# Optimization experiments

Hardware: AMD Instinct MI355X
Metric: run time of the kernel (lower is better)

Reference implementation:

```python
import jax, jax.numpy as jnp
import numpy as np

B, N, D = 4, 2048, 1024
H, HD = 16, 64
S = 11  # n_scales
D4 = jnp.array([0.4829629131445341, 0.8365163037378079,
                0.2241438680420134, -0.1294095225512604], dtype=jnp.float32)


def _causal_dilated_d4(f, d):
    """Causal depthwise D4 conv with dilation d along axis 2. f: [B,H,N,HD].
    Matches torch F.pad(x,(3d,0)) + F.conv1d(dilation=d, groups=C):
    y[n] = sum_t D4[t] * f[n - (3-t)*d]."""
    n = f.shape[2]
    fp = jnp.pad(f, ((0, 0), (0, 0), (3 * d, 0), (0, 0)))
    return (D4[0] * fp[:, :, 0:n, :]
            + D4[1] * fp[:, :, d:d + n, :]
            + D4[2] * fp[:, :, 2 * d:2 * d + n, :]
            + D4[3] * fp[:, :, 3 * d:3 * d + n, :])


def setup_inputs() -> dict:
    key = jax.random.key(0)
    ks = jax.random.split(key, 10)
    s = 0.02
    return {
        "x": jax.random.normal(ks[0], (B, N, D), dtype=jnp.float32),
        "Wqkv": jax.random.normal(ks[1], (3 * D, D), dtype=jnp.float32) * s,
        "bqkv": jnp.zeros((3 * D,), dtype=jnp.float32),
        "Wo": jax.random.normal(ks[2], (D, D), dtype=jnp.float32) * s,
        "bo": jnp.zeros((D,), dtype=jnp.float32),
        "Wg": jax.random.normal(ks[3], (D, D), dtype=jnp.float32) * s,
        "bg": jnp.full((D,), 2.0, dtype=jnp.float32),
        "scale_gain": jnp.zeros((S, H), dtype=jnp.float32),
        "Wqs": jax.random.normal(ks[4], (S, HD), dtype=jnp.float32) * 0.01,
        "field_coupling": jnp.eye(H, dtype=jnp.float32)
        + 0.01 * jax.random.normal(ks[5], (H, H), dtype=jnp.float32),
    }


def reference(x, Wqkv, bqkv, Wo, bo, Wg, bg, scale_gain, Wqs, field_coupling):
    b, n, d = x.shape
    qkv = x @ Wqkv.T + bqkv                          # [B,N,3D]
    q, k, v = jnp.split(qkv, 3, axis=-1)
    q = q.reshape(b, n, H, HD).transpose(0, 2, 1, 3)  # [B,H,N,HD]
    k = k.reshape(b, n, H, HD).transpose(0, 2, 1, 3)
    v = v.reshape(b, n, H, HD).transpose(0, 2, 1, 3)

    # per-position scale gains: learned prior + query-conditioned offset
    q_offset = jnp.einsum('bhnd,sd->bhns', q, Wqs)    # [B,H,N,S]
    prior = scale_gain.T[None, :, None, :]            # [1,H,1,S]
    gains = jax.nn.softmax(q_offset + prior, axis=-1)

    # deposit: field[i] = V[i] * ||K[i]||
    k_mag = jnp.linalg.norm(k, axis=-1, keepdims=True)
    field = v * k_mag                                 # [B,H,N,HD]

    # propagate: causal multiscale dilated D4 conv, gain-weighted accumulate
    out_field = jnp.zeros_like(field)
    for j in range(S):
        y = _causal_dilated_d4(field, 1 << j)
        out_field = out_field + gains[:, :, :, j:j + 1] * y

    coupling = jax.nn.softmax(field_coupling, axis=-1)
    out_field = jnp.einsum('ij,bjnd->bind', coupling, out_field)

    gate = jax.nn.sigmoid(x @ Wg.T + bg)              # [B,N,D]
    gathered = out_field.transpose(0, 2, 1, 3).reshape(b, n, d)
    return (gathered * gate) @ Wo.T + bo
```

## Files before the change

kernel.cpp:

```cpp
#include <hip/hip_runtime.h>
#include <hip/hip_bf16.h>
#include <stdint.h>
#include <math.h>

#define BB 4
#define NN 2048
#define DD 1024
#define HH 16
#define HDD 64
#define SS 11

#define D4_0 0.4829629131445341f
#define D4_1 0.8365163037378079f
#define D4_2 0.2241438680420134f
#define D4_3 (-0.1294095225512604f)

typedef __bf16 bf16_t;
typedef __bf16 bf16x4_t __attribute__((ext_vector_type(4)));
typedef __bf16 bf16x8_t __attribute__((ext_vector_type(8)));
typedef float f32x4_t __attribute__((ext_vector_type(4)));

__global__ __launch_bounds__(256) void cvt_all_k(const float* __restrict__ s0,
                                                 const float* __restrict__ s1,
                                                 const float* __restrict__ s2,
                                                 const float* __restrict__ s3,
                                                 bf16_t* __restrict__ d0,
                                                 bf16_t* __restrict__ d1,
                                                 bf16_t* __restrict__ d2,
                                                 bf16_t* __restrict__ d3) {
  const int n0 = 2097152, n1 = 786432, n2 = 262144, n3 = 262144;
  int i = blockIdx.x * 256 + threadIdx.x;
  const float* s;
  bf16_t* d;
  if (i < n0) { s = s0; d = d0; }
  else if (i < n0 + n1) { i -= n0; s = s1; d = d1; }
  else if (i < n0 + n1 + n2) { i -= n0 + n1; s = s2; d = d2; }
  else { i -= n0 + n1 + n2; if (i >= n3) return; s = s3; d = d3; }
  f32x4_t v = ((const f32x4_t*)s)[i];
  bf16x4_t o;
  o[0] = (bf16_t)v[0]; o[1] = (bf16_t)v[1]; o[2] = (bf16_t)v[2]; o[3] = (bf16_t)v[3];
  ((bf16x4_t*)d)[i] = o;
}

__device__ __forceinline__ void gload16(const void* g, void* l) {
  __builtin_amdgcn_global_load_lds((__attribute__((address_space(1))) void*)(void*)g,
                                   (__attribute__((address_space(3))) void*)l,
                                   16, 0, 0);
}

__global__ __launch_bounds__(512, 2) void gemm256(const bf16_t* __restrict__ Aa,
                                                  const bf16_t* __restrict__ Bw,
                                                  const float* __restrict__ bias0,
                                                  const float* __restrict__ bias1,
                                                  bf16_t* __restrict__ out0,
                                                  bf16_t* __restrict__ out1) {
  __shared__ bf16_t sA[2][16384];
  __shared__ bf16_t sB[2][16384];

  const int tid = threadIdx.x;
  const int s = (blockIdx.x & 7) * 64 + (blockIdx.x >> 3);
  const int mtile = s >> 4;
  const int ntile = s & 15;
  const int row0 = mtile << 8;
  const int col0 = ntile << 8;

  const int w = tid >> 6, lane = tid & 63;
  const int wm = w >> 2, wn = w & 3;
  const int wmbase = wm << 7;
  const int wnbase = wn << 6;
  const int m16 = lane & 15, quad = lane >> 4;

  f32x4_t acc[8][4];
#pragma unroll
  for (int i = 0; i < 8; i++)
#pragma unroll
    for (int jq = 0; jq < 4; jq++) acc[i][jq] = (f32x4_t){0.f, 0.f, 0.f, 0.f};

  auto stage_half = [&](int buf, int tensor, int half, int t) {
    if (t >= 16) return;
    const bf16_t* gb = tensor ? Bw : Aa;
    const int gr0 = (tensor ? col0 : row0) + (half << 7);
    const int kb = t << 6;
    bf16_t* lbase = (tensor ? sB[buf] : sA[buf]) + (half << 13);
#pragma unroll
    for (int l = 0; l < 2; ++l) {
      int c = l * 512 + tid;
      int row = c >> 3, kc = c & 7;
      int swz = kc ^ (row & 7);
      const bf16_t* g = gb + (size_t)(gr0 + row) * 1024 + kb + swz * 8;
      bf16_t* lp = lbase + ((l * 512 + (tid & 448)) << 3);
      gload16(g, lp);
    }
  };

  bf16x8_t af[4], bfr[4];
  auto rdA = [&](int buf, int ih, int ks) {
#pragma unroll
    for (int i = 0; i < 4; i++) {
      int ar = wmbase + ((ih * 4 + i) << 4) + m16;
      int kc = (ks << 2) + quad;
      af[i] = *(const bf16x8_t*)&sA[buf][ar * 64 + ((kc ^ (ar & 7)) << 3)];
    }
  };
  auto rdB = [&](int buf, int ks) {
#pragma unroll
    for (int jq = 0; jq < 4; jq++) {
      int br = wnbase + (jq << 4) + m16;
      int kc = (ks << 2) + quad;
      bfr[jq] = *(const bf16x8_t*)&sB[buf][br * 64 + ((kc ^ (br & 7)) << 3)];
    }
  };
  auto domfma = [&](int ih) {
#pragma unroll
    for (int i = 0; i < 4; i++)
#pragma unroll
      for (int jq = 0; jq < 4; jq++)
        acc[ih * 4 + i][jq] =
            __builtin_amdgcn_mfma_f32_16x16x32_bf16(af[i], bfr[jq], acc[ih * 4 + i][jq], 0, 0, 0);
  };

#define PH_ENTER()                                        \
  __builtin_amdgcn_s_barrier();                           \
  asm volatile("s_waitcnt lgkmcnt(0)" ::: "memory");      \
  __builtin_amdgcn_sched_barrier(0);                      \
  __builtin_amdgcn_s_setprio(1)
#define PH_EXIT()                                         \
  __builtin_amdgcn_s_setprio(0);                          \
  __builtin_amdgcn_s_barrier()
#define PH_EXIT_V4()                                      \
  __builtin_amdgcn_s_setprio(0);                          \
  asm volatile("s_waitcnt vmcnt(4)" ::: "memory");        \
  __builtin_amdgcn_s_barrier()
#define PH_EXIT_V0()                                      \
  __builtin_amdgcn_s_setprio(0);                          \
  asm volatile("s_waitcnt vmcnt(0)" ::: "memory");        \
  __builtin_amdgcn_s_barrier()

  stage_half(0, 0, 0, 0); stage_half(0, 0, 1, 0);
  stage_half(0, 1, 0, 0); stage_half(0, 1, 1, 0);
  stage_half(1, 1, 0, 1); stage_half(1, 1, 1, 1);
  asm volatile("s_waitcnt vmcnt(4)" ::: "memory");
  __builtin_amdgcn_s_barrier();

  for (int it = 0; it < 8; ++it) {
    const int Tb = 2 * it + 1, T2 = 2 * it + 2, T3 = 2 * it + 3;
    rdA(0, 0, 0); rdB(0, 0);
    stage_half(1, 0, 0, Tb); stage_half(1, 0, 1, Tb);
    PH_ENTER(); domfma(0); PH_EXIT();
    rdA(0, 1, 0);
    PH_ENTER(); domfma(1); PH_EXIT();
    rdA(0, 0, 1); rdB(0, 1);
    PH_ENTER(); domfma(0); PH_EXIT();
    rdA(0, 1, 1);
    stage_half(0, 1, 0, T2); stage_half(0, 1, 1, T2);
    PH_ENTER(); domfma(1);
    if (T2 < 16) { PH_EXIT_V4(); } else { PH_EXIT_V0(); }
    rdA(1, 0, 0); rdB(1, 0);
    stage_half(0, 0, 0, T2); stage_half(0, 0, 1, T2);
    PH_ENTER(); domfma(0); PH_EXIT();
    rdA(1, 1, 0);
    PH_ENTER(); domfma(1); PH_EXIT();
    rdA(1, 0, 1); rdB(1, 1);
    PH_ENTER(); domfma(0); PH_EXIT();
    rdA(1, 1, 1);
    stage_half(1, 1, 0, T3); stage_half(1, 1, 1, T3);
    PH_ENTER(); domfma(1);
    if (T3 < 16) { PH_EXIT_V4(); } else { PH_EXIT_V0(); }
  }
#undef PH_ENTER
#undef PH_EXIT
#undef PH_EXIT_V4
#undef PH_EXIT_V0

  const bool is_gate = (col0 >= 3072);
#pragma unroll
  for (int i = 0; i < 8; i++) {
#pragma unroll
    for (int jq = 0; jq < 4; jq++) {
      const int grow0 = row0 + wmbase + (i << 4) + (quad << 2);
      const int gcol = col0 + wnbase + (jq << 4) + m16;
      const float bval = is_gate ? bias1[gcol - 3072] : bias0[gcol];
#pragma unroll
      for (int r = 0; r < 4; r++) {
        float val = acc[i][jq][r] + bval;
        if (is_gate)
          out1[(size_t)(grow0 + r) * 1024 + (gcol - 3072)] =
              (bf16_t)(1.f / (1.f + __expf(-val)));
        else
          out0[(size_t)(grow0 + r) * 3072 + gcol] = (bf16_t)val;
      }
    }
  }
}

template <int MODE>
__global__ __launch_bounds__(256) void gemm_nt(const bf16_t* __restrict__ A,
                                               const bf16_t* __restrict__ Bw,
                                               const float* __restrict__ bias0,
                                               const float* __restrict__ bias1,
                                               void* __restrict__ out0v,
                                               void* __restrict__ out1v,
                                               int M, int Nn, int K) {
  __shared__ bf16_t As[128 * 64];
  __shared__ bf16_t Bs[128 * 64];

  const int tid = threadIdx.x;
  const int ntiles = Nn >> 7;
  const int grp = ntiles << 3;
  const int g = blockIdx.x / grp;
  const int j = blockIdx.x % grp;
  const int mtile = (g << 3) | (j & 7);
  const int ntile = j >> 3;
  const int row0 = mtile << 7;
  const int col0 = ntile << 7;
  const int w = tid >> 6, lane = tid & 63;
  const int wm = w >> 1, wn = w & 1;
  const int m16 = lane & 15, quad = lane >> 4;

  f32x4_t acc[4][4];
#pragma unroll
  for (int i = 0; i < 4; i++)
#pragma unroll
    for (int jj = 0; jj < 4; jj++) acc[i][jj] = (f32x4_t){0.f, 0.f, 0.f, 0.f};

  for (int kb = 0; kb < K; kb += 64) {
    __syncthreads();
#pragma unroll
    for (int r = 0; r < 4; ++r) {
      int c = r * 256 + tid;
      int row = c >> 3, kc = c & 7;
      int swz = kc ^ (row & 7);
      const bf16_t* gpA = A + (size_t)(row0 + row) * K + kb + swz * 8;
      const bf16_t* gpB = Bw + (size_t)(col0 + row) * K + kb + swz * 8;
      bf16_t* lpA = As + (size_t)(r * 256 + (tid & 192)) * 8;
      bf16_t* lpB = Bs + (size_t)(r * 256 + (tid & 192)) * 8;
      gload16(gpA, lpA);
      gload16(gpB, lpB);
    }
    __syncthreads();

#pragma unroll
    for (int kk = 0; kk < 2; ++kk) {
      bf16x8_t af[4], bfr[4];
      const int kc = (kk << 2) + quad;
#pragma unroll
      for (int i = 0; i < 4; i++) {
        int arow = (wm << 6) + (i << 4) + m16;
        af[i] = *(const bf16x8_t*)(As + arow * 64 + ((kc ^ (arow & 7)) << 3));
        int brow = (wn << 6) + (i << 4) + m16;
        bfr[i] = *(const bf16x8_t*)(Bs + brow * 64 + ((kc ^ (brow & 7)) << 3));
      }
#pragma unroll
      for (int i = 0; i < 4; i++)
#pragma unroll
        for (int jj = 0; jj < 4; jj++)
          acc[i][jj] = __builtin_amdgcn_mfma_f32_16x16x32_bf16(af[i], bfr[jj], acc[i][jj], 0, 0, 0);
    }
  }

#pragma unroll
  for (int i = 0; i < 4; i++) {
#pragma unroll
    for (int jj = 0; jj < 4; jj++) {
      const int grow0 = row0 + (wm << 6) + (i << 4) + (quad << 2);
      const int gcol = col0 + (wn << 6) + (jj << 4) + m16;
      const float bval = (MODE == 0)
                             ? (gcol < 3072 ? bias0[gcol] : bias1[gcol - 3072])
                             : bias0[gcol];
#pragma unroll
      for (int r = 0; r < 4; r++) {
        float val = acc[i][jj][r] + bval;
        if (MODE == 0) {
          if (gcol < 3072)
            ((bf16_t*)out0v)[(size_t)(grow0 + r) * 3072 + gcol] = (bf16_t)val;
          else
            ((bf16_t*)out1v)[(size_t)(grow0 + r) * 1024 + (gcol - 3072)] =
                (bf16_t)(1.f / (1.f + __expf(-val)));
        } else {
          ((float*)out0v)[(size_t)(grow0 + r) * Nn + gcol] = val;
        }
      }
    }
  }
}

__global__ __launch_bounds__(256) void field_gains_k(const bf16_t* __restrict__ qkvb,
                                                     const float* __restrict__ scale_gain,
                                                     const float* __restrict__ Wqs,
                                                     bf16_t* __restrict__ fieldb,
                                                     float* __restrict__ gains) {
  __shared__ float skmag[4 * 16];
  const int tid = threadIdx.x;
  const int w = tid >> 6, lane = tid & 63;
  const int bn = blockIdx.x * 4 + w;
  const int b = bn >> 11, n_pos = bn & 2047;
  const int m16 = lane & 15, quad = lane >> 4;
  const bf16_t* qp = qkvb + (size_t)bn * 3072;

  bf16x8_t aq[2], ak[2], bw[2];
#pragma unroll
  for (int it = 0; it < 2; it++) {
    const int koff = it * 32 + quad * 8;
    aq[it] = *(const bf16x8_t*)(qp + m16 * 64 + koff);
    ak[it] = *(const bf16x8_t*)(qp + 1024 + m16 * 64 + koff);
    bf16x8_t bwv;
    if (m16 < SS) {
      const float* wp = Wqs + m16 * 64 + koff;
#pragma unroll
      for (int j = 0; j < 8; j++) bwv[j] = (bf16_t)wp[j];
    } else {
#pragma unroll
      for (int j = 0; j < 8; j++) bwv[j] = (bf16_t)0.f;
    }
    bw[it] = bwv;
  }

  f32x4_t acc_l = (f32x4_t){0.f, 0.f, 0.f, 0.f};
  f32x4_t acc_k = (f32x4_t){0.f, 0.f, 0.f, 0.f};
#pragma unroll
  for (int it = 0; it < 2; it++) {
    acc_l = __builtin_amdgcn_mfma_f32_16x16x32_bf16(aq[it], bw[it], acc_l, 0, 0, 0);
    acc_k = __builtin_amdgcn_mfma_f32_16x16x32_bf16(ak[it], ak[it], acc_k, 0, 0, 0);
  }

#pragma unroll
  for (int r = 0; r < 4; r++) {
    if (m16 == quad * 4 + r) skmag[w * 16 + m16] = sqrtf(fmaxf(acc_k[r], 0.f));
  }

#pragma unroll
  for (int r = 0; r < 4; r++) {
    const int m = quad * 4 + r;
    float lg = (m16 < SS) ? (acc_l[r] + scale_gain[m16 * 16 + m]) : -1e30f;
    float mx = lg;
#pragma unroll
    for (int sh = 1; sh < 16; sh <<= 1) mx = fmaxf(mx, __shfl_xor(mx, sh, 64));
    float e = (m16 < SS) ? __expf(lg - mx) : 0.f;
    float se = e;
#pragma unroll
    for (int sh = 1; sh < 16; sh <<= 1) se += __shfl_xor(se, sh, 64);
    if (m16 < SS)
      gains[((size_t)(b * 16 + m) * 2048 + n_pos) * SS + m16] = e / se;
  }

  __syncthreads();

#pragma unroll
  for (int h = 0; h < 16; h++) {
    const float km = skmag[w * 16 + h];
    const float v = (float)qp[2048 + h * 64 + lane];
    fieldb[((size_t)(b * 16 + h) * 2048 + n_pos) * 64 + lane] = (bf16_t)(v * km);
  }
}

__global__ __launch_bounds__(256) void conv_k(const bf16_t* __restrict__ field,
                                              const float* __restrict__ gains,
                                              bf16_t* __restrict__ facc) {
  __shared__ float sg[32 * SS];
  const int tid = threadIdx.x;
  const int blk = blockIdx.x;
  const int bh = blk & 63;
  const int ntile = blk >> 6;
  const int n0 = ntile * 32;

  for (int i = tid; i < 32 * SS; i += 256)
    sg[i] = gains[((size_t)bh * 2048 + n0) * SS + i];
  __syncthreads();

  const int w = tid >> 6, lane = tid & 63;
  const int nsub = lane >> 3, c = lane & 7;
  const int ln = w * 8 + nsub;
  const int n = n0 + ln;
  const bf16_t* frow = field + (size_t)bh * 2048 * 64;

  float g[SS];
#pragma unroll
  for (int s = 0; s < SS; s++) g[s] = sg[ln * SS + s];

  float acc[8];
  {
    bf16x8_t f0 = *(const bf16x8_t*)(frow + (size_t)n * 64 + c * 8);
#pragma unroll
    for (int q = 0; q < 8; q++) acc[q] = D4_3 * (float)f0[q];
  }
#pragma unroll
  for (int j = 0; j < 11; j++) {
    float wgt = D4_2 * g[j];
    if (j >= 1) wgt += D4_1 * g[j - 1];
    int rr = n - (1 << j);
    float wv = rr >= 0 ? wgt : 0.f;
    rr = rr >= 0 ? rr : 0;
    bf16x8_t fv = *(const bf16x8_t*)(frow + (size_t)rr * 64 + c * 8);
#pragma unroll
    for (int q = 0; q < 8; q++) acc[q] += wv * (float)fv[q];
  }
#pragma unroll
  for (int j = 0; j < 10; j++) {
    int rr = n - (3 << j);
    float wv = rr >= 0 ? (D4_0 * g[j]) : 0.f;
    rr = rr >= 0 ? rr : 0;
    bf16x8_t fv = *(const bf16x8_t*)(frow + (size_t)rr * 64 + c * 8);
#pragma unroll
    for (int q = 0; q < 8; q++) acc[q] += wv * (float)fv[q];
  }
  bf16x8_t o;
#pragma unroll
  for (int q = 0; q < 8; q++) o[q] = (bf16_t)acc[q];
  *(bf16x8_t*)(facc + ((size_t)bh * 2048 + n) * 64 + c * 8) = o;
}

__global__ __launch_bounds__(1024) void couple_gate_k(const bf16_t* __restrict__ facc,
                                                      const float* __restrict__ fcoup,
                                                      const bf16_t* __restrict__ gate,
                                                      bf16_t* __restrict__ gmat) {
  __shared__ float sacc[1024];
  __shared__ float sc[256];
  __shared__ float scn[256];
  const int tid = threadIdx.x;
  const int bn = blockIdx.x;
  const int b = bn >> 11, n = bn & 2047;
  if (tid < 256) sc[tid] = fcoup[tid];
  const int i = tid >> 6, hd = tid & 63;
  sacc[tid] = (float)facc[(((size_t)(b * 16 + i)) * 2048 + n) * 64 + hd];
  __syncthreads();
  if (tid < 16) {
    float row[16];
    float mx = -1e30f;
#pragma unroll
    for (int j = 0; j < 16; j++) { row[j] = sc[tid * 16 + j]; mx = fmaxf(mx, row[j]); }
    float se = 0.f;
#pragma unroll
    for (int j = 0; j < 16; j++) { row[j] = __expf(row[j] - mx); se += row[j]; }
    float inv = 1.f / se;
#pragma unroll
    for (int j = 0; j < 16; j++) scn[tid * 16 + j] = row[j] * inv;
  }
  __syncthreads();
  float s = 0.f;
#pragma unroll
  for (int j = 0; j < 16; j++) s += scn[i * 16 + j] * sacc[j * 64 + hd];
  const float gt = (float)gate[(size_t)bn * 1024 + tid];
  gmat[(size_t)bn * 1024 + tid] = (bf16_t)(s * gt);
}

extern "C" void kernel_launch(void* const* d_in, const int* in_sizes, int n_in,
                              void* d_out, int out_size, void* d_ws, size_t ws_size,
                              hipStream_t stream) {
  (void)in_sizes; (void)n_in; (void)out_size; (void)ws_size;
  const float* x = (const float*)d_in[0];
  const float* Wqkv = (const float*)d_in[1];
  const float* bqkv = (const float*)d_in[2];
  const float* Wo = (const float*)d_in[3];
  const float* bo = (const float*)d_in[4];
  const float* Wg = (const float*)d_in[5];
  const float* bg = (const float*)d_in[6];
  const float* scale_gain = (const float*)d_in[7];
  const float* Wqs = (const float*)d_in[8];
  const float* fcoup = (const float*)d_in[9];

  char* ws = (char*)d_ws;
  size_t off = 0;
  auto alloc = [&](size_t bytes) {
    void* p = ws + off;
    off += (bytes + 255) & ~(size_t)255;
    return p;
  };
  bf16_t* xb = (bf16_t*)alloc(8192ull * 1024 * 2);
  bf16_t* Wab = (bf16_t*)alloc(4096ull * 1024 * 2);
  bf16_t* Wob = (bf16_t*)alloc(1024ull * 1024 * 2);
  bf16_t* qkvb = (bf16_t*)alloc(8192ull * 3072 * 2);
  bf16_t* gateb = (bf16_t*)alloc(8192ull * 1024 * 2);
  bf16_t* fieldb = (bf16_t*)alloc(8388608ull * 2);
  float* gains = (float*)alloc(8192ull * 16 * SS * 4);
  bf16_t* facc = (bf16_t*)alloc(8388608ull * 2);
  bf16_t* gmat = (bf16_t*)alloc(8192ull * 1024 * 2);

  cvt_all_k<<<13316, 256, 0, stream>>>(x, Wqkv, Wg, Wo,
                                       xb, Wab, Wab + 3072ull * 1024, Wob);

  gemm256<<<512, 512, 0, stream>>>(xb, Wab, bqkv, bg, qkvb, gateb);

  field_gains_k<<<2048, 256, 0, stream>>>(qkvb, scale_gain, Wqs, fieldb, gains);

  conv_k<<<4096, 256, 0, stream>>>(fieldb, gains, facc);

  couple_gate_k<<<8192, 1024, 0, stream>>>(facc, fcoup, gateb, gmat);

  gemm_nt<1><<<64 * 8, 256, 0, stream>>>(gmat, Wob, bo, nullptr, (void*)d_out, nullptr, 8192, 1024, 1024);
}
```

Measured before the change: 275.3 us.

## Double-buffer MFMA operand registers to overlap LDS reads with compute

The GEMM main loop now holds two register banks of A/B fragments. The next phase's LDS reads are issued before the current phase's MFMAs, with partial lgkmcnt waits (4/8) instead of full drains, so shared-memory read latency is hidden behind matrix math. The global-load wait is changed to vmcnt(0) at fixed points. This raises VGPR pressure, which could reduce occupancy or cause spills, and the tuned waitcnt counts carry correctness risk if the instruction ordering shifts.

After: 285.3 us. 1.04x slower.

```diff
diff --git a/kernel.cpp b/kernel.cpp
--- a/kernel.cpp
+++ b/kernel.cpp
@@ -93,84 +93,81 @@
     }
   };
 
-  bf16x8_t af[4], bfr[4];
-  auto rdA = [&](int buf, int ih, int ks) {
+  bf16x8_t bA[2][4], bB[2][4];
+  auto rdA = [&](int bank, int buf, int ih, int ks) {
 #pragma unroll
     for (int i = 0; i < 4; i++) {
       int ar = wmbase + ((ih * 4 + i) << 4) + m16;
       int kc = (ks << 2) + quad;
-      af[i] = *(const bf16x8_t*)&sA[buf][ar * 64 + ((kc ^ (ar & 7)) << 3)];
+      bA[bank][i] = *(const bf16x8_t*)&sA[buf][ar * 64 + ((kc ^ (ar & 7)) << 3)];
     }
   };
-  auto rdB = [&](int buf, int ks) {
+  auto rdB = [&](int bank, int buf, int ks) {
 #pragma unroll
     for (int jq = 0; jq < 4; jq++) {
       int br = wnbase + (jq << 4) + m16;
       int kc = (ks << 2) + quad;
-      bfr[jq] = *(const bf16x8_t*)&sB[buf][br * 64 + ((kc ^ (br & 7)) << 3)];
+      bB[bank][jq] = *(const bf16x8_t*)&sB[buf][br * 64 + ((kc ^ (br & 7)) << 3)];
     }
   };
-  auto domfma = [&](int ih) {
+  auto domfma = [&](int ab, int bb, int ih) {
 #pragma unroll
     for (int i = 0; i < 4; i++)
 #pragma unroll
       for (int jq = 0; jq < 4; jq++)
         acc[ih * 4 + i][jq] =
-            __builtin_amdgcn_mfma_f32_16x16x32_bf16(af[i], bfr[jq], acc[ih * 4 + i][jq], 0, 0, 0);
+            __builtin_amdgcn_mfma_f32_16x16x32_bf16(bA[ab][i], bB[bb][jq], acc[ih * 4 + i][jq], 0, 0, 0);
   };
 
-#define PH_ENTER()                                        \
-  __builtin_amdgcn_s_barrier();                           \
-  asm volatile("s_waitcnt lgkmcnt(0)" ::: "memory");      \
-  __builtin_amdgcn_sched_barrier(0);                      \
-  __builtin_amdgcn_s_setprio(1)
-#define PH_EXIT()                                         \
-  __builtin_amdgcn_s_setprio(0);                          \
-  __builtin_amdgcn_s_barrier()
-#define PH_EXIT_V4()                                      \
-  __builtin_amdgcn_s_setprio(0);                          \
-  asm volatile("s_waitcnt vmcnt(4)" ::: "memory");        \
-  __builtin_amdgcn_s_barrier()
-#define PH_EXIT_V0()                                      \
-  __builtin_amdgcn_s_setprio(0);                          \
-  asm volatile("s_waitcnt vmcnt(0)" ::: "memory");        \
-  __builtin_amdgcn_s_barrier()
+#define BAR() __builtin_amdgcn_s_barrier()
+#define WAITL4() asm volatile("s_waitcnt lgkmcnt(4)" ::: "memory"); __builtin_amdgcn_sched_barrier(0)
+#define WAITL8() asm volatile("s_waitcnt lgkmcnt(8)" ::: "memory"); __builtin_amdgcn_sched_barrier(0)
+#define WAITL0() asm volatile("s_waitcnt lgkmcnt(0)" ::: "memory"); __builtin_amdgcn_sched_barrier(0)
+#define PRIO1() __builtin_amdgcn_s_setprio(1)
+#define PRIO0() __builtin_amdgcn_s_setprio(0)
+#define WAITV0() asm volatile("s_waitcnt vmcnt(0)" ::: "memory")
 
   stage_half(0, 0, 0, 0); stage_half(0, 0, 1, 0);
   stage_half(0, 1, 0, 0); stage_half(0, 1, 1, 0);
   stage_half(1, 1, 0, 1); stage_half(1, 1, 1, 1);
   asm volatile("s_waitcnt vmcnt(4)" ::: "memory");
-  __builtin_amdgcn_s_barrier();
+  BAR();
+  rdA(0, 0, 0, 0); rdB(0, 0, 0);
+  WAITL0();
 
   for (int it = 0; it < 8; ++it) {
     const int Tb = 2 * it + 1, T2 = 2 * it + 2, T3 = 2 * it + 3;
-    rdA(0, 0, 0); rdB(0, 0);
+    const bool lastit = (it == 7);
+    rdA(1, 0, 1, 0);
     stage_half(1, 0, 0, Tb); stage_half(1, 0, 1, Tb);
-    PH_ENTER(); domfma(0); PH_EXIT();
-    rdA(0, 1, 0);
-    PH_ENTER(); domfma(1); PH_EXIT();
-    rdA(0, 0, 1); rdB(0, 1);
-    PH_ENTER(); domfma(0); PH_EXIT();
-    rdA(0, 1, 1);
+    BAR(); WAITL4(); PRIO1(); domfma(0, 0, 0); PRIO0(); BAR();
+    rdA(0, 0, 0, 1); rdB(1, 0, 1);
+    BAR(); WAITL8(); PRIO1(); domfma(1, 0, 1); PRIO0(); BAR();
+    rdA(1, 0, 1, 1);
+    BAR(); WAITL4(); PRIO1(); domfma(0, 1, 0); PRIO0(); WAITV0(); BAR();
+    rdA(0, 1, 0, 0); rdB(0, 1, 0);
     stage_half(0, 1, 0, T2); stage_half(0, 1, 1, T2);
-    PH_ENTER(); domfma(1);
-    if (T2 < 16) { PH_EXIT_V4(); } else { PH_EXIT_V0(); }
-    rdA(1, 0, 0); rdB(1, 0);
+    BAR(); WAITL8(); PRIO1(); domfma(1, 1, 1); PRIO0(); BAR();
+    rdA(1, 1, 1, 0);
     stage_half(0, 0, 0, T2); stage_half(0, 0, 1, T2);
-    PH_ENTER(); domfma(0); PH_EXIT();
-    rdA(1, 1, 0);
-    PH_ENTER(); domfma(1); PH_EXIT();
-    rdA(1, 0, 1); rdB(1, 1);
-    PH_ENTER(); domfma(0); PH_EXIT();
-    rdA(1, 1, 1);
+    BAR(); WAITL4(); PRIO1(); domfma(0, 0, 0); PRIO0(); BAR();
+    rdA(0, 1, 0, 1); rdB(1, 1, 1);
+    BAR(); WAITL8(); PRIO1(); domfma(1, 0, 1); PRIO0(); BAR();
+    rdA(1, 1, 1, 1);
+    BAR(); WAITL4(); PRIO1(); domfma(0, 1, 0); PRIO0(); WAITV0(); BAR();
+    if (!lastit) { rdA(0, 0, 0, 0); rdB(0, 0, 0); }
     stage_half(1, 1, 0, T3); stage_half(1, 1, 1, T3);
-    PH_ENTER(); domfma(1);
-    if (T3 < 16) { PH_EXIT_V4(); } else { PH_EXIT_V0(); }
-  }
-#undef PH_ENTER
-#undef PH_EXIT
-#undef PH_EXIT_V4
-#undef PH_EXIT_V0
+    BAR();
+    if (!lastit) { WAITL8(); } else { WAITL0(); }
+    PRIO1(); domfma(1, 1, 1); PRIO0(); BAR();
+  }
+#undef BAR
+#undef WAITL4
+#undef WAITL8
+#undef WAITL0
+#undef PRIO1
+#undef PRIO0
+#undef WAITV0
 
   const bool is_gate = (col0 >= 3072);
 #pragma unroll
```

## Fuse dilated conv with head coupling and gating into one kernel

Applied to the files above, without the earlier changes.

Merges the multiscale causal conv kernel and the head-coupling/gate kernel into a single kernel. Each 1024-thread block handles 16 positions across all 16 heads, keeps the conv output in shared memory, then applies the coupling softmax and gate with vectorized bf16x8 accesses. This removes the facc intermediate write and read and one kernel launch, and replaces 8192 small blocks with 512. The grid is much smaller, so fewer blocks are available to hide the latency of the scattered field loads.

After: 265.2 us, median of 2. 3.7% less time.

```diff
diff --git a/kernel.cpp b/kernel.cpp
--- a/kernel.cpp
+++ b/kernel.cpp
@@ -353,81 +353,24 @@
   }
 }
 
-__global__ __launch_bounds__(256) void conv_k(const bf16_t* __restrict__ field,
-                                              const float* __restrict__ gains,
-                                              bf16_t* __restrict__ facc) {
-  __shared__ float sg[32 * SS];
-  const int tid = threadIdx.x;
-  const int blk = blockIdx.x;
-  const int bh = blk & 63;
-  const int ntile = blk >> 6;
-  const int n0 = ntile * 32;
-
-  for (int i = tid; i < 32 * SS; i += 256)
-    sg[i] = gains[((size_t)bh * 2048 + n0) * SS + i];
-  __syncthreads();
-
-  const int w = tid >> 6, lane = tid & 63;
-  const int nsub = lane >> 3, c = lane & 7;
-  const int ln = w * 8 + nsub;
-  const int n = n0 + ln;
-  const bf16_t* frow = field + (size_t)bh * 2048 * 64;
-
-  float g[SS];
-#pragma unroll
-  for (int s = 0; s < SS; s++) g[s] = sg[ln * SS + s];
-
-  float acc[8];
-  {
-    bf16x8_t f0 = *(const bf16x8_t*)(frow + (size_t)n * 64 + c * 8);
-#pragma unroll
-    for (int q = 0; q < 8; q++) acc[q] = D4_3 * (float)f0[q];
-  }
-#pragma unroll
-  for (int j = 0; j < 11; j++) {
-    float wgt = D4_2 * g[j];
-    if (j >= 1) wgt += D4_1 * g[j - 1];
-    int rr = n - (1 << j);
-    float wv = rr >= 0 ? wgt : 0.f;
-    rr = rr >= 0 ? rr : 0;
-    bf16x8_t fv = *(const bf16x8_t*)(frow + (size_t)rr * 64 + c * 8);
-#pragma unroll
-    for (int q = 0; q < 8; q++) acc[q] += wv * (float)fv[q];
-  }
-#pragma unroll
-  for (int j = 0; j < 10; j++) {
-    int rr = n - (3 << j);
-    float wv = rr >= 0 ? (D4_0 * g[j]) : 0.f;
-    rr = rr >= 0 ? rr : 0;
-    bf16x8_t fv = *(const bf16x8_t*)(frow + (size_t)rr * 64 + c * 8);
-#pragma unroll
-    for (int q = 0; q < 8; q++) acc[q] += wv * (float)fv[q];
-  }
-  bf16x8_t o;
-#pragma unroll
-  for (int q = 0; q < 8; q++) o[q] = (bf16_t)acc[q];
-  *(bf16x8_t*)(facc + ((size_t)bh * 2048 + n) * 64 + c * 8) = o;
-}
-
-__global__ __launch_bounds__(1024) void couple_gate_k(const bf16_t* __restrict__ facc,
+__global__ __launch_bounds__(1024) void conv_couple_k(const bf16_t* __restrict__ field,
+                                                      const float* __restrict__ gains,
                                                       const float* __restrict__ fcoup,
                                                       const bf16_t* __restrict__ gate,
                                                       bf16_t* __restrict__ gmat) {
-  __shared__ float sacc[1024];
-  __shared__ float sc[256];
+  __shared__ bf16_t fld[16 * 16 * 64];
   __shared__ float scn[256];
   const int tid = threadIdx.x;
-  const int bn = blockIdx.x;
-  const int b = bn >> 11, n = bn & 2047;
-  if (tid < 256) sc[tid] = fcoup[tid];
-  const int i = tid >> 6, hd = tid & 63;
-  sacc[tid] = (float)facc[(((size_t)(b * 16 + i)) * 2048 + n) * 64 + hd];
-  __syncthreads();
+  const int blk = blockIdx.x;
+  const int b = blk >> 7;
+  const int nt = blk & 127;
+  const int n0 = nt * 16;
+
   if (tid < 16) {
     float row[16];
     float mx = -1e30f;
 #pragma unroll
-    for (int j = 0; j < 16; j++) { row[j] = sc[tid * 16 + j]; mx = fmaxf(mx, row[j]); }
+    for (int j = 0; j < 16; j++) { row[j] = fcoup[tid * 16 + j]; mx = fmaxf(mx, row[j]); }
     float se = 0.f;
 #pragma unroll
     for (int j = 0; j < 16; j++) { row[j] = __expf(row[j] - mx); se += row[j]; }
@@ -435,12 +378,75 @@
 #pragma unroll
     for (int j = 0; j < 16; j++) scn[tid * 16 + j] = row[j] * inv;
   }
+
+  const int w = tid >> 6, lane = tid & 63;
+  const int nsub = lane >> 3, c = lane & 7;
+  const bf16_t* frow = field + ((size_t)(b * 16 + w)) * 2048 * 64;
+
+#pragma unroll
+  for (int p = 0; p < 2; ++p) {
+    const int nl = p * 8 + nsub;
+    const int n = n0 + nl;
+    float g[SS];
+    const float* gp = gains + ((size_t)(b * 16 + w) * 2048 + n) * SS;
+#pragma unroll
+    for (int s = 0; s < SS; s++) g[s] = gp[s];
+
+    float acc[8];
+    {
+      bf16x8_t f0 = *(const bf16x8_t*)(frow + (size_t)n * 64 + c * 8);
+#pragma unroll
+      for (int q = 0; q < 8; q++) acc[q] = D4_3 * (float)f0[q];
+    }
+#pragma unroll
+    for (int j = 0; j < 11; j++) {
+      float wgt = D4_2 * g[j];
+      if (j >= 1) wgt += D4_1 * g[j - 1];
+      int rr = n - (1 << j);
+      float wv = rr >= 0 ? wgt : 0.f;
+      rr = rr >= 0 ? rr : 0;
+      bf16x8_t fv = *(const bf16x8_t*)(frow + (size_t)rr * 64 + c * 8);
+#pragma unroll
+      for (int q = 0; q < 8; q++) acc[q] += wv * (float)fv[q];
+    }
+#pragma unroll
+    for (int j = 0; j < 10; j++) {
+      int rr = n - (3 << j);
+      float wv = rr >= 0 ? (D4_0 * g[j]) : 0.f;
+      rr = rr >= 0 ? rr : 0;
+      bf16x8_t fv = *(const bf16x8_t*)(frow + (size_t)rr * 64 + c * 8);
+#pragma unroll
+      for (int q = 0; q < 8; q++) acc[q] += wv * (float)fv[q];
+    }
+    bf16x8_t o;
+#pragma unroll
+    for (int q = 0; q < 8; q++) o[q] = (bf16_t)acc[q];
+    *(bf16x8_t*)&fld[w * 1024 + nl * 64 + c * 8] = o;
+  }
+
   __syncthreads();
-  float s = 0.f;
-#pragma unroll
-  for (int j = 0; j < 16; j++) s += scn[i * 16 + j] * sacc[j * 64 + hd];
-  const float gt = (float)gate[(size_t)bn * 1024 + tid];
-  gmat[(size_t)bn * 1024 + tid] = (bf16_t)(s * gt);
+
+#pragma unroll
+  for (int p = 0; p < 2; ++p) {
+    const int nl = p * 8 + nsub;
+    const int n = n0 + nl;
+    float s8[8];
+#pragma unroll
+    for (int q = 0; q < 8; q++) s8[q] = 0.f;
+#pragma unroll
+    for (int j = 0; j < 16; j++) {
+      const float cw = scn[w * 16 + j];
+      bf16x8_t v = *(const bf16x8_t*)&fld[j * 1024 + nl * 64 + c * 8];
+#pragma unroll
+      for (int q = 0; q < 8; q++) s8[q] += cw * (float)v[q];
+    }
+    const size_t base = ((size_t)(b * 2048 + n)) * 1024 + w * 64 + c * 8;
+    bf16x8_t gt = *(const bf16x8_t*)(gate + base);
+    bf16x8_t o;
+#pragma unroll
+    for (int q = 0; q < 8; q++) o[q] = (bf16_t)(s8[q] * (float)gt[q]);
+    *(bf16x8_t*)(gmat + base) = o;
+  }
 }
 
 extern "C" void kernel_launch(void* const* d_in, const int* in_sizes, int n_in,
@@ -472,7 +478,6 @@
   bf16_t* gateb = (bf16_t*)alloc(8192ull * 1024 * 2);
   bf16_t* fieldb = (bf16_t*)alloc(8388608ull * 2);
   float* gains = (float*)alloc(8192ull * 16 * SS * 4);
-  bf16_t* facc = (bf16_t*)alloc(8388608ull * 2);
   bf16_t* gmat = (bf16_t*)alloc(8192ull * 1024 * 2);
 
   cvt_all_k<<<13316, 256, 0, stream>>>(x, Wqkv, Wg, Wo,
@@ -482,9 +487,7 @@
 
   field_gains_k<<<2048, 256, 0, stream>>>(qkvb, scale_gain, Wqs, fieldb, gains);
 
-  conv_k<<<4096, 256, 0, stream>>>(fieldb, gains, facc);
-
-  couple_gate_k<<<8192, 1024, 0, stream>>>(facc, fcoup, gateb, gmat);
+  conv_couple_k<<<512, 1024, 0, stream>>>(fieldb, gains, fcoup, gateb, gmat);
 
   gemm_nt<1><<<64 * 8, 256, 0, stream>>>(gmat, Wob, bo, nullptr, (void*)d_out, nullptr, 8192, 1024, 1024);
 }
```
